# Optimization experiments

Hardware: AMD Instinct MI355X
Metric: run time of the kernel (lower is better)

## Reference

```python
import jax, jax.numpy as jnp
import numpy as np
from jax import lax

B = 2; C = 256; NH = 8; NP = 4; NUM_LAYERS = 6; FFN = 1024
IN_SIZES = (512, 1024, 2048)
LVL_SHAPES = ((64, 64), (32, 32), (16, 16), (8, 8), (4, 4))
NL = len(LVL_SHAPES); DH = C // NH
N = sum(h * w for h, w in LVL_SHAPES)  # 5456 tokens over the pyramid


def _ln(x, g, b):
    m = x.mean(-1, keepdims=True)
    v = x.var(-1, keepdims=True)
    return (x - m) * lax.rsqrt(v + 1e-5) * g + b


def _gn(x, g, b, groups=8):
    Bb, Cc, Hh, Ww = x.shape
    xr = x.reshape(Bb, groups, Cc // groups, Hh, Ww)
    m = xr.mean((2, 3, 4), keepdims=True)
    v = xr.var((2, 3, 4), keepdims=True)
    xr = (xr - m) * lax.rsqrt(v + 1e-5)
    return xr.reshape(Bb, Cc, Hh, Ww) * g[None, :, None, None] + b[None, :, None, None]


def _conv(x, w, b, stride, pad):
    y = lax.conv_general_dilated(x, w, (stride, stride), [(pad, pad), (pad, pad)],
                                 dimension_numbers=('NCHW', 'OIHW', 'NCHW'))
    return y + b[None, :, None, None]


def _priors():
    # normalized (cx, cy) anchor centers per pyramid location
    pr = []
    for (fh, fw) in LVL_SHAPES:
        cy = (jnp.arange(fh, dtype=jnp.float32) + 0.5) / fh
        cx = (jnp.arange(fw, dtype=jnp.float32) + 0.5) / fw
        gy, gx = jnp.meshgrid(cy, cx, indexing='ij')
        pr.append(jnp.stack([gx, gy], -1).reshape(-1, 2))
    return jnp.concatenate(pr, 0)  # [N,2]


def _sample(vl, loc, fh, fw):
    # vl: [B,NH,S_l,DH] flattened level values; loc: [B,N,NH,NP,2] in [0,1]
    x = loc[..., 0] * fw - 0.5
    y = loc[..., 1] * fh - 0.5
    x0 = jnp.floor(x); y0 = jnp.floor(y)
    lx = x - x0; ly = y - y0

    def gather(xi, yi):
        inb = ((xi >= 0) & (xi <= fw - 1) & (yi >= 0) & (yi <= fh - 1)).astype(vl.dtype)
        xc = jnp.clip(xi, 0, fw - 1).astype(jnp.int32)
        yc = jnp.clip(yi, 0, fh - 1).astype(jnp.int32)
        idx = (yc * fw + xc).transpose(0, 2, 1, 3).reshape(B, NH, N * NP)
        g = jnp.take_along_axis(vl, idx[..., None], axis=2)  # [B,NH,N*NP,DH]
        g = g.reshape(B, NH, N, NP, DH).transpose(0, 2, 1, 3, 4)  # [B,N,NH,NP,DH]
        return g * inb[..., None]

    return (gather(x0, y0) * ((1 - lx) * (1 - ly))[..., None]
            + gather(x0 + 1, y0) * (lx * (1 - ly))[..., None]
            + gather(x0, y0 + 1) * ((1 - lx) * ly)[..., None]
            + gather(x0 + 1, y0 + 1) * (lx * ly)[..., None])


def _attn_layer(x, priors, g1, b1_, woff, boff, watt, batt, wval, bval, wout, bout):
    q = _ln(x, g1, b1_)
    off = (q @ woff + boff).reshape(B, N, NH, NL, NP, 2)
    att = jax.nn.softmax((q @ watt + batt).reshape(B, N, NH, NL * NP), axis=-1)
    att = att.reshape(B, N, NH, NL, NP)
    val = (q @ wval + bval).reshape(B, N, NH, DH)
    normz = jnp.array([[w, h] for (h, w) in LVL_SHAPES], jnp.float32)  # (W,H) per level
    loc = priors[None, :, None, None, None, :] + off / normz[None, None, None, :, None, :]
    out = jnp.zeros((B, N, NH, DH), x.dtype)
    start = 0
    for l, (fh, fw) in enumerate(LVL_SHAPES):
        vl = val[:, start:start + fh * fw].transpose(0, 2, 1, 3)  # [B,NH,S_l,DH]
        s = _sample(vl, loc[:, :, :, l], fh, fw)  # [B,N,NH,NP,DH]
        out = out + (s * att[:, :, :, l, :, None]).sum(3)
        start += fh * fw
    return x + out.reshape(B, N, C) @ wout + bout


def _ffn(x, g2, b2_, w1, b1_, w2, b2_2):
    h = jax.nn.relu(_ln(x, g2, b2_) @ w1 + b1_)
    return x + h @ w2 + b2_2


def _forward(in_map0, in_map1, in_map2, pw0, pb0, pw1, pb1, pw2, pb2,
             buw0, bub0, gng, gnb, buw1, bub1,
             ln1g, ln1b, woff, boff, watt, batt, wval, bval, wout, bout,
             ln2g, ln2b, w1, b1, w2, b2):
    maps = [_conv(in_map0, pw0, pb0, 1, 0), _conv(in_map1, pw1, pb1, 1, 0), _conv(in_map2, pw2, pb2, 1, 0)]
    m = _conv(in_map2, buw0, bub0, 2, 1)  # bottom-up from raw C5 (2048ch)
    maps.append(m)
    m = _conv(jax.nn.relu(_gn(m, gng, gnb)), buw1, bub1, 2, 1)
    maps.append(m)
    feats = jnp.concatenate([mm.reshape(B, C, -1).transpose(0, 2, 1) for mm in maps], axis=1)  # [B,N,C]
    priors = _priors()
    for i in range(NUM_LAYERS):
        feats = _attn_layer(feats, priors, ln1g[i], ln1b[i], woff[i], boff[i],
                            watt[i], batt[i], wval[i], bval[i], wout[i], bout[i])
        feats = _ffn(feats, ln2g[i], ln2b[i], w1[i], b1[i], w2[i], b2[i])
    return feats


def setup_inputs():
    key = jax.random.key(0)
    ks = list(jax.random.split(key, 40)); ki = iter(ks)
    def rn(shape, s=0.02):
        return jax.random.normal(next(ki), shape, jnp.float32) * s
    inp = {}
    for i, (cs, (h, w)) in enumerate(zip(IN_SIZES, LVL_SHAPES[:3])):
        inp[f"in_map{i}"] = jax.random.normal(next(ki), (B, cs, h, w), jnp.float32)
    for i, cs in enumerate(IN_SIZES):
        inp[f"pw{i}"] = rn((C, cs, 1, 1)); inp[f"pb{i}"] = jnp.zeros((C,), jnp.float32)
    inp["buw0"] = rn((C, IN_SIZES[-1], 3, 3)); inp["bub0"] = jnp.zeros((C,), jnp.float32)
    inp["gng"] = jnp.ones((C,), jnp.float32); inp["gnb"] = jnp.zeros((C,), jnp.float32)
    inp["buw1"] = rn((C, C, 3, 3)); inp["bub1"] = jnp.zeros((C,), jnp.float32)
    LYR = NUM_LAYERS
    inp["ln1g"] = jnp.ones((LYR, C), jnp.float32); inp["ln1b"] = jnp.zeros((LYR, C), jnp.float32)
    inp["woff"] = rn((LYR, C, NH * NL * NP * 2), 0.01)
    th = np.arange(NH) * (2.0 * np.pi / NH)
    grid = np.stack([np.cos(th), np.sin(th)], -1)
    grid = grid / np.abs(grid).max(-1, keepdims=True)  # [NH,2]
    boff = np.tile(grid[:, None, None, :], (1, NL, NP, 1)) * (np.arange(NP) + 1)[None, None, :, None]
    inp["boff"] = jnp.tile(jnp.asarray(boff.reshape(-1), jnp.float32)[None], (LYR, 1))
    inp["watt"] = rn((LYR, C, NH * NL * NP), 0.01); inp["batt"] = jnp.zeros((LYR, NH * NL * NP), jnp.float32)
    inp["wval"] = rn((LYR, C, C)); inp["bval"] = jnp.zeros((LYR, C), jnp.float32)
    inp["wout"] = rn((LYR, C, C)); inp["bout"] = jnp.zeros((LYR, C), jnp.float32)
    inp["ln2g"] = jnp.ones((LYR, C), jnp.float32); inp["ln2b"] = jnp.zeros((LYR, C), jnp.float32)
    inp["w1"] = rn((LYR, C, FFN)); inp["b1"] = jnp.zeros((LYR, FFN), jnp.float32)
    inp["w2"] = rn((LYR, FFN, C)); inp["b2"] = jnp.zeros((LYR, C), jnp.float32)
    return inp


def reference(in_map0, in_map1, in_map2, pw0, pb0, pw1, pb1, pw2, pb2,
              buw0, bub0, gng, gnb, buw1, bub1,
              ln1g, ln1b, woff, boff, watt, batt, wval, bval, wout, bout,
              ln2g, ln2b, w1, b1, w2, b2):
    feats = _forward(in_map0, in_map1, in_map2, pw0, pb0, pw1, pb1, pw2, pb2,
                     buw0, bub0, gng, gnb, buw1, bub1,
                     ln1g, ln1b, woff, boff, watt, batt, wval, bval, wout, bout,
                     ln2g, ln2b, w1, b1, w2, b2)
    outs = []
    start = 0
    for (fh, fw) in LVL_SHAPES:
        outs.append(feats[:, start:start + fh * fw].transpose(0, 2, 1).reshape(B, C, fh, fw))
        start += fh * fw
    return tuple(outs)
```

## Files before the change

### kernel.cpp

```cpp
#include <hip/hip_runtime.h>
#include <cstdint>

typedef long long i64;
typedef unsigned short u16;
typedef __attribute__((ext_vector_type(8))) short short8;
typedef __attribute__((ext_vector_type(8))) unsigned short us8;
typedef __attribute__((ext_vector_type(4))) float f32x4;

#define NTOK 5456
#define BNROWS 10912
#define NLAYERS 6

__device__ __forceinline__ u16 f2bf(float f) {
  unsigned u = __float_as_uint(f);
  return (u16)((u + 0x7FFFu + ((u >> 16) & 1u)) >> 16);
}
__device__ __forceinline__ float bf2f(u16 h) {
  return __uint_as_float(((unsigned)h) << 16);
}

template<int BNT>
__global__ __launch_bounds__(256) void mgemm_k(
    const u16* __restrict__ A, const u16* __restrict__ B, int K,
    float* __restrict__ C, float* __restrict__ C2, u16* __restrict__ C16, i64 sCm,
    const float* __restrict__ bias, int relu, int addres, int qkv,
    int M, int N, int mbsh, i64 bCz,
    int KS, float* __restrict__ part)
{
  constexpr int NW = BNT / 32;
  __shared__ u16 Asm[2][128 * 64];
  __shared__ u16 Bsm[2][BNT * 64];
  int tid = threadIdx.x;

  int bx = blockIdx.x, by = blockIdx.y;
  int gx = gridDim.x, gy = gridDim.y;
  int nwg = gx * gy;
  if (KS == 1 && nwg >= 16) {
    int lin = bx + gx * by;
    int xcd = lin & 7, k = lin >> 3;
    int q = nwg >> 3, r = nwg & 7;
    int f = (xcd < r) ? (xcd * (q + 1) + k) : (r * (q + 1) + (xcd - r) * q + k);
    bx = f / gy;
    by = f - bx * gy;
  }
  int m0 = bx * 128, n0 = by * BNT;

  int ks = blockIdx.z;
  int Kc = K / KS;
  int k0 = ks * Kc;
  int lane = tid & 63, w = tid >> 6;
  int wr = w >> 1, wc = w & 1;
  int r16 = lane & 15, g = lane >> 4;

  f32x4 acc[4][NW];
#pragma unroll
  for (int mi = 0; mi < 4; mi++)
#pragma unroll
    for (int nj = 0; nj < NW; nj++) acc[mi][nj] = (f32x4){0.f, 0.f, 0.f, 0.f};

  const u16* Ag = A + (i64)m0 * K + k0;
  const u16* Bg = B + (i64)n0 * K + k0;
  int nt = Kc >> 6;

  auto stage = [&](int buf, int kt) {
#pragma unroll
    for (int r = 0; r < 4; r++) {
      int s = r * 256 + tid;
      int row = s >> 3, c = s & 7;
      int cs = ((c ^ (row & 7)) << 3);
      __builtin_amdgcn_global_load_lds(
          (const __attribute__((address_space(1))) void*)(Ag + (i64)row * K + kt + cs),
          (__attribute__((address_space(3))) void*)(&Asm[buf][(r * 256 + (w << 6)) << 3]),
          16, 0, 0);
    }
#pragma unroll
    for (int r = 0; r < NW; r++) {
      int s = r * 256 + tid;
      int row = s >> 3, c = s & 7;
      int cs = ((c ^ (row & 7)) << 3);
      __builtin_amdgcn_global_load_lds(
          (const __attribute__((address_space(1))) void*)(Bg + (i64)row * K + kt + cs),
          (__attribute__((address_space(3))) void*)(&Bsm[buf][(r * 256 + (w << 6)) << 3]),
          16, 0, 0);
    }
  };

  stage(0, 0);
  __syncthreads();
  for (int t = 0; t < nt; t++) {
    int cur = t & 1;
    if (t + 1 < nt) stage(cur ^ 1, (t + 1) << 6);
#pragma unroll
    for (int h = 0; h < 2; h++) {
      short8 av[4], bv[NW];
#pragma unroll
      for (int mi = 0; mi < 4; mi++) {
        int row = wr * 64 + mi * 16 + r16;
        av[mi] = *(const short8*)&Asm[cur][row * 64 + ((((h << 2) + g) ^ (row & 7)) << 3)];
      }
#pragma unroll
      for (int nj = 0; nj < NW; nj++) {
        int row = wc * (NW * 16) + nj * 16 + r16;
        bv[nj] = *(const short8*)&Bsm[cur][row * 64 + ((((h << 2) + g) ^ (row & 7)) << 3)];
      }
#pragma unroll
      for (int mi = 0; mi < 4; mi++)
#pragma unroll
        for (int nj = 0; nj < NW; nj++)
          acc[mi][nj] = __builtin_amdgcn_mfma_f32_16x16x32_bf16(
              av[mi], bv[nj], acc[mi][nj], 0, 0, 0);
    }
    __syncthreads();
  }

  if (KS > 1) {
#pragma unroll
    for (int mi = 0; mi < 4; mi++)
#pragma unroll
      for (int nj = 0; nj < NW; nj++)
#pragma unroll
        for (int r = 0; r < 4; r++) {
          int grow = m0 + wr * 64 + mi * 16 + g * 4 + r;
          int gcol = n0 + wc * (NW * 16) + nj * 16 + r16;
          if (grow < M) part[((i64)ks * M + grow) * N + gcol] = acc[mi][nj][r];
        }
  } else if (qkv) {
    u16* off16 = (u16*)C;
    u16* att16 = (u16*)C2;
#pragma unroll
    for (int mi = 0; mi < 4; mi++)
#pragma unroll
      for (int nj = 0; nj < NW; nj++)
#pragma unroll
        for (int r = 0; r < 4; r++) {
          int grow = m0 + wr * 64 + mi * 16 + g * 4 + r;
          int gcol = n0 + wc * (NW * 16) + nj * 16 + r16;
          if (grow < M) {
            float v = acc[mi][nj][r] + bias[gcol];
            if (gcol < 320) off16[(i64)grow * 320 + gcol] = f2bf(v);
            else if (gcol < 480) att16[(i64)grow * 160 + (gcol - 320)] = f2bf(v);
            else if (gcol < 736) C16[(i64)grow * 256 + (gcol - 480)] = f2bf(v);
          }
        }
  } else {
    float bv[NW];
    int gc0 = n0 + wc * (NW * 16) + r16;
#pragma unroll
    for (int nj = 0; nj < NW; nj++)
      bv[nj] = bias ? bias[gc0 + nj * 16] : 0.f;
    int mask = (1 << mbsh) - 1;
#pragma unroll
    for (int mi = 0; mi < 4; mi++) {
#pragma unroll
      for (int r = 0; r < 4; r++) {
        int grow = m0 + wr * 64 + mi * 16 + g * 4 + r;
        if (grow >= M) continue;
        i64 rowb = (i64)(grow >> mbsh) * bCz + (i64)(grow & mask) * sCm;
#pragma unroll
        for (int nj = 0; nj < NW; nj++) {
          int gcol = gc0 + nj * 16;
          if (gcol >= N) continue;
          float v = acc[mi][nj][r] + bv[nj];
          if (relu) v = fmaxf(v, 0.f);
          i64 ci = rowb + gcol;
          if (C16) C16[ci] = f2bf(v);
          else {
            if (addres) v += C[ci];
            C[ci] = v;
          }
        }
      }
    }
  }
}

__global__ __launch_bounds__(512, 1) void ffn_fused_k(
    float* __restrict__ feats, const u16* __restrict__ w1n,
    const u16* __restrict__ w2n, const float* __restrict__ b1,
    const float* __restrict__ b2, const float* __restrict__ lng,
    const float* __restrict__ lnb, int M)
{
  __shared__ u16 B1s[2][64 * 256];
  __shared__ u16 B2s[2][256 * 64];
  __shared__ u16 Hs[64 * 88];
  __shared__ float b1s[1024];
  u16* As = &B1s[1][0];

  int tid = threadIdx.x;
  int lane = tid & 63, w = tid >> 6;
  int wr = w >> 1, wc = w & 1;
  int r16 = lane & 15, g = lane >> 4;
  int m0 = blockIdx.x * 64;

  auto stageW = [&](int buf, int ch) {
#pragma unroll
    for (int r = 0; r < 4; r++) {
      int s = r * 512 + tid;
      int row = s >> 5, c = s & 31;
      int cs = ((c ^ (row & 7)) << 3);
      __builtin_amdgcn_global_load_lds(
          (const __attribute__((address_space(1))) void*)(w1n + (i64)(ch * 64 + row) * 256 + cs),
          (__attribute__((address_space(3))) void*)(&B1s[buf][(r * 512 + (w << 6)) << 3]),
          16, 0, 0);
    }
#pragma unroll
    for (int r = 0; r < 4; r++) {
      int s = r * 512 + tid;
      int row = s >> 3, c = s & 7;
      int cs = ((c ^ (row & 7)) << 3);
      __builtin_amdgcn_global_load_lds(
          (const __attribute__((address_space(1))) void*)(w2n + (i64)row * 1024 + ch * 64 + cs),
          (__attribute__((address_space(3))) void*)(&B2s[buf][(r * 512 + (w << 6)) << 3]),
          16, 0, 0);
    }
  };

  stageW(0, 0);
  for (int i = tid; i < 1024; i += 512) b1s[i] = b1[i];

  {
    int rw = tid >> 3, c0 = (tid & 7) * 32;
    const float* fr = feats + (i64)(m0 + rw) * 256 + c0;
    float4 x[8];
    float s = 0.f, ss = 0.f;
#pragma unroll
    for (int j = 0; j < 8; j++) {
      x[j] = ((const float4*)fr)[j];
      s += x[j].x + x[j].y + x[j].z + x[j].w;
      ss += x[j].x * x[j].x + x[j].y * x[j].y + x[j].z * x[j].z + x[j].w * x[j].w;
    }
#pragma unroll
    for (int o = 1; o <= 4; o <<= 1) { s += __shfl_xor(s, o); ss += __shfl_xor(ss, o); }
    float mean = s * (1.f / 256.f);
    float rs = rsqrtf(ss * (1.f / 256.f) - mean * mean + 1e-5f);
    const float4* gp = (const float4*)(lng + c0);
    const float4* bp = (const float4*)(lnb + c0);
#pragma unroll
    for (int j = 0; j < 8; j += 2) {
      float4 g0 = gp[j], g1 = gp[j + 1];
      float4 b0 = bp[j], b1_ = bp[j + 1];
      us8 o;
      o[0] = f2bf((x[j].x - mean) * rs * g0.x + b0.x);
      o[1] = f2bf((x[j].y - mean) * rs * g0.y + b0.y);
      o[2] = f2bf((x[j].z - mean) * rs * g0.z + b0.z);
      o[3] = f2bf((x[j].w - mean) * rs * g0.w + b0.w);
      o[4] = f2bf((x[j + 1].x - mean) * rs * g1.x + b1_.x);
      o[5] = f2bf((x[j + 1].y - mean) * rs * g1.y + b1_.y);
      o[6] = f2bf((x[j + 1].z - mean) * rs * g1.z + b1_.z);
      o[7] = f2bf((x[j + 1].w - mean) * rs * g1.w + b1_.w);
      int gr = (tid & 7) * 4 + (j >> 1);
      *(us8*)&As[rw * 256 + ((gr ^ (rw & 7)) << 3)] = o;
    }
  }
  __syncthreads();

  short8 av_all[8];
  {
    int row = wr * 16 + r16;
#pragma unroll
    for (int ks = 0; ks < 8; ks++)
      av_all[ks] = *(const short8*)&As[row * 256 + (((ks * 4 + g) ^ (row & 7)) << 3)];
  }
  __syncthreads();

  f32x4 acc2[8];
#pragma unroll
  for (int nj = 0; nj < 8; nj++) acc2[nj] = (f32x4){0.f, 0.f, 0.f, 0.f};

  int cur = 0;
  for (int ch = 0; ch < 16; ch++) {
    if (ch + 1 < 16) stageW(cur ^ 1, ch + 1);

    f32x4 acc1[2];
#pragma unroll
    for (int nj = 0; nj < 2; nj++) acc1[nj] = (f32x4){0.f, 0.f, 0.f, 0.f};
#pragma unroll
    for (int ks = 0; ks < 8; ks++) {
      short8 bv[2];
#pragma unroll
      for (int nj = 0; nj < 2; nj++) {
        int row = wc * 32 + nj * 16 + r16;
        bv[nj] = *(const short8*)&B1s[cur][row * 256 + (((ks * 4 + g) ^ (row & 7)) << 3)];
      }
#pragma unroll
      for (int nj = 0; nj < 2; nj++)
        acc1[nj] = __builtin_amdgcn_mfma_f32_16x16x32_bf16(
            av_all[ks], bv[nj], acc1[nj], 0, 0, 0);
    }
#pragma unroll
    for (int nj = 0; nj < 2; nj++)
#pragma unroll
      for (int r = 0; r < 4; r++) {
        int hr = wr * 16 + g * 4 + r;
        int hc = wc * 32 + nj * 16 + r16;
        float v = acc1[nj][r] + b1s[ch * 64 + hc];
        Hs[hr * 88 + hc] = f2bf(fmaxf(v, 0.f));
      }
    __syncthreads();

#pragma unroll
    for (int hh = 0; hh < 2; hh++) {
      short8 av2 = *(const short8*)&Hs[(wr * 16 + r16) * 88 + hh * 32 + g * 8];
      short8 bv2[8];
#pragma unroll
      for (int nj = 0; nj < 8; nj++) {
        int n = wc * 128 + nj * 16 + r16;
        bv2[nj] = *(const short8*)&B2s[cur][n * 64 + (((hh * 4 + g) ^ (n & 7)) << 3)];
      }
#pragma unroll
      for (int nj = 0; nj < 8; nj++)
        acc2[nj] = __builtin_amdgcn_mfma_f32_16x16x32_bf16(
            av2, bv2[nj], acc2[nj], 0, 0, 0);
    }
    __syncthreads();
    cur ^= 1;
  }

#pragma unroll
  for (int r = 0; r < 4; r++) {
    int grow = m0 + wr * 16 + g * 4 + r;
    if (grow >= M) continue;
#pragma unroll
    for (int nj = 0; nj < 8; nj++) {
      int col = wc * 128 + nj * 16 + r16;
      i64 ci = (i64)grow * 256 + col;
      feats[ci] += acc2[nj][r] + b2[col];
    }
  }
}

__global__ void reduce_k(const float* __restrict__ part, float* __restrict__ C,
    const float* __restrict__ bias, int mbsh, i64 bCz, i64 sCm, int M, int N, int KS)
{
  int idx = blockIdx.x * 256 + threadIdx.x;
  if (idx >= M * N) return;
  int m = idx / N, n = idx - m * N;
  float v = bias ? bias[n] : 0.f;
  for (int ks = 0; ks < KS; ks++) v += part[((i64)ks * M + m) * N + n];
  C[(i64)(m >> mbsh) * bCz + (i64)(m & ((1 << mbsh) - 1)) * sCm + n] = v;
}

__global__ void cvt_w_pro_k(const float* __restrict__ pw0, const float* __restrict__ pw1,
    const float* __restrict__ pw2, const float* __restrict__ buw0,
    const float* __restrict__ buw1, u16* __restrict__ dst)
{
  int idx = blockIdx.x * 256 + threadIdx.x;
  if (idx >= 6225920) return;
  float v;
  if (idx < 131072) v = pw0[idx];
  else if (idx < 393216) v = pw1[idx - 131072];
  else if (idx < 917504) v = pw2[idx - 393216];
  else if (idx < 5636096) v = buw0[idx - 917504];
  else v = buw1[idx - 5636096];
  dst[idx] = f2bf(v);
}

__global__ void cvt_w_layer_k(const float* __restrict__ woff, const float* __restrict__ watt,
    const float* __restrict__ wval, const float* __restrict__ wout,
    const float* __restrict__ w1, const float* __restrict__ w2, u16* __restrict__ dst)
{
  int L = blockIdx.y;
  int o = blockIdx.x * 256 + threadIdx.x;
  if (o >= 786432) return;
  u16* d = dst + (i64)L * 786432;
  float v;
  if (o < 196608) {
    int n = o >> 8, k = o & 255;
    if (n < 320) v = woff[(i64)L * 81920 + k * 320 + n];
    else if (n < 480) v = watt[(i64)L * 40960 + k * 160 + (n - 320)];
    else if (n < 736) v = wval[(i64)L * 65536 + k * 256 + (n - 480)];
    else v = 0.f;
  } else if (o < 262144) {
    int o2 = o - 196608; int n = o2 >> 8, k = o2 & 255;
    v = wout[(i64)L * 65536 + k * 256 + n];
  } else if (o < 524288) {
    int o2 = o - 262144; int n = o2 >> 8, k = o2 & 255;
    v = w1[(i64)L * 262144 + (i64)k * 1024 + n];
  } else {
    int o2 = o - 524288; int n = o2 >> 10, k = o2 & 1023;
    v = w2[(i64)L * 262144 + (i64)k * 256 + n];
  }
  d[o] = f2bf(v);
}

__global__ void cvt_bias_k(const float* __restrict__ boff, const float* __restrict__ batt,
    const float* __restrict__ bval, float* __restrict__ bq)
{
  int idx = blockIdx.x * 256 + threadIdx.x;
  if (idx >= NLAYERS * 768) return;
  int L = idx / 768, n = idx - L * 768;
  float v;
  if (n < 320) v = boff[(i64)L * 320 + n];
  else if (n < 480) v = batt[(i64)L * 160 + (n - 320)];
  else if (n < 736) v = bval[(i64)L * 256 + (n - 480)];
  else v = 0.f;
  bq[idx] = v;
}

__global__ __launch_bounds__(256) void trans_cvt_k(const float* __restrict__ in,
    u16* __restrict__ out, int K, int P)
{
  __shared__ float tile[32][33];
  int p0 = blockIdx.x * 32, k0 = blockIdx.y * 32, b = blockIdx.z;
  int tx = threadIdx.x & 31, ty = threadIdx.x >> 5;
  const float* ib = in + (i64)b * K * P;
  for (int i = ty; i < 32; i += 8)
    tile[i][tx] = ib[(i64)(k0 + i) * P + p0 + tx];
  __syncthreads();
  for (int i = ty; i < 32; i += 8)
    out[((i64)b * P + p0 + i) * K + k0 + tx] = f2bf(tile[tx][i]);
}

__global__ void im2col_bf16_k(const float* __restrict__ in, u16* __restrict__ out,
    int Cin, int Hin, int Win, int Ho, int Wo)
{
  int Kk = Cin * 9;
  i64 total = (i64)2 * Ho * Wo * Kk;
  i64 o = (i64)blockIdx.x * 256 + threadIdx.x;
  if (o >= total) return;
  int k = (int)(o % Kk);
  int m = (int)(o / Kk);
  int hw = Ho * Wo;
  int b = m / hw, pix = m - b * hw;
  int oy = pix / Wo, ox = pix - oy * Wo;
  int ci = k / 9, r = k - ci * 9;
  int ky = r / 3, kx = r - ky * 3;
  int iy = oy * 2 - 1 + ky, ix = ox * 2 - 1 + kx;
  float v = 0.f;
  if (iy >= 0 && iy < Hin && ix >= 0 && ix < Win)
    v = in[(((i64)b * Cin + ci) * Hin + iy) * Win + ix];
  out[o] = f2bf(v);
}

__global__ void gn_relu_k(const float* __restrict__ feats, float* __restrict__ y,
    const float* __restrict__ g, const float* __restrict__ bt)
{
  int grp = blockIdx.x, b = blockIdx.y;
  int tid = threadIdx.x;
  const float* fb = feats + ((i64)b * NTOK + 5376) * 256 + grp * 32;
  float s = 0.f, ss = 0.f;
  for (int i = tid; i < 2048; i += 256) {
    int cl = i >> 6, p = i & 63;
    float v = fb[(i64)p * 256 + cl];
    s += v; ss += v * v;
  }
  __shared__ float sb[4], ssb[4];
#pragma unroll
  for (int o = 32; o > 0; o >>= 1) { s += __shfl_down(s, o); ss += __shfl_down(ss, o); }
  int wv = tid >> 6;
  if ((tid & 63) == 0) { sb[wv] = s; ssb[wv] = ss; }
  __syncthreads();
  float ts = sb[0] + sb[1] + sb[2] + sb[3];
  float tss = ssb[0] + ssb[1] + ssb[2] + ssb[3];
  float mean = ts * (1.f / 2048.f);
  float rs = rsqrtf(tss * (1.f / 2048.f) - mean * mean + 1e-5f);
  for (int i = tid; i < 2048; i += 256) {
    int cl = i >> 6, p = i & 63;
    int c = grp * 32 + cl;
    float v = (fb[(i64)p * 256 + cl] - mean) * rs * g[c] + bt[c];
    y[((i64)b * 256 + c) * 64 + p] = fmaxf(v, 0.f);
  }
}

__global__ __launch_bounds__(256) void ln_k(const float* __restrict__ x,
    u16* __restrict__ y, const float* __restrict__ g, const float* __restrict__ bt,
    int rows)
{
  int row = blockIdx.x * 4 + (threadIdx.x >> 6);
  if (row >= rows) return;
  int lane = threadIdx.x & 63;
  float4 v = ((const float4*)(x + (i64)row * 256))[lane];
  float s = v.x + v.y + v.z + v.w;
  float ss = v.x * v.x + v.y * v.y + v.z * v.z + v.w * v.w;
#pragma unroll
  for (int o = 32; o > 0; o >>= 1) { s += __shfl_down(s, o); ss += __shfl_down(ss, o); }
  s = __shfl(s, 0);
  ss = __shfl(ss, 0);
  float mean = s * (1.f / 256.f);
  float rs = rsqrtf(ss * (1.f / 256.f) - mean * mean + 1e-5f);
  float4 gg = ((const float4*)g)[lane];
  float4 bb = ((const float4*)bt)[lane];
  ushort4 o4;
  o4.x = f2bf((v.x - mean) * rs * gg.x + bb.x);
  o4.y = f2bf((v.y - mean) * rs * gg.y + bb.y);
  o4.z = f2bf((v.z - mean) * rs * gg.z + bb.z);
  o4.w = f2bf((v.w - mean) * rs * gg.w + bb.w);
  ((ushort4*)(y + (i64)row * 256))[lane] = o4;
}

__global__ __launch_bounds__(256) void dsample_k(
    const u16* __restrict__ val, const u16* __restrict__ off,
    const u16* __restrict__ att, u16* __restrict__ out)
{
  const int FH[5] = {64, 32, 16, 8, 4};
  const int ST[5] = {0, 4096, 5120, 5376, 5440};
  int bid = blockIdx.x;
  int chunk = (bid & 7) * 86 + (bid >> 3);
  if (chunk >= 682) return;
  int lane = threadIdx.x & 63;
  int half = lane >> 5;
  int l32 = lane & 31;
  int t = chunk * 8 + ((threadIdx.x >> 6) << 1) + half;
  int b = blockIdx.y;
  int h = l32 >> 2, d4 = l32 & 3;

  int lv;
  if (t < 4096)      lv = 0;
  else if (t < 5120) lv = 1;
  else if (t < 5376) lv = 2;
  else if (t < 5440) lv = 3;
  else               lv = 4;
  int loc = t - ST[lv];
  int sh = 6 - lv;
  int py = loc >> sh, px = loc - (py << sh);
  float inv = 1.f / (float)FH[lv];
  float prx = (px + 0.5f) * inv, pry = (py + 0.5f) * inv;
  i64 bt = (i64)b * NTOK + t;
  const u16* offp = off + bt * 320 + h * 40;
  const u16* attp = att + bt * 160 + h * 20;
  const u16* vbase = val + ((i64)b * NTOK) * 256 + h * 32 + d4 * 8;

  float own_a[5], own_fx[5], own_fy[5];
  int own_pk[5];
  float mx = -1e30f;
#pragma unroll
  for (int j = 0; j < 5; j++) {
    float lg = bf2f(attp[d4 + 4 * j]);
    own_a[j] = lg;
    mx = fmaxf(mx, lg);
  }
  mx = fmaxf(mx, __shfl_xor(mx, 1));
  mx = fmaxf(mx, __shfl_xor(mx, 2));
  float sum = 0.f;
#pragma unroll
  for (int j = 0; j < 5; j++) {
    float e = __expf(own_a[j] - mx);
    own_a[j] = e;
    sum += e;
  }
  sum += __shfl_xor(sum, 1);
  sum += __shfl_xor(sum, 2);
  float rinv = 1.f / sum;
#pragma unroll
  for (int j = 0; j < 5; j++) {
    int p = d4 + 4 * j;
    own_a[j] *= rinv;
    unsigned opk = *(const unsigned*)(offp + 2 * p);
    float ox = bf2f((u16)(opk & 0xFFFF));
    float oy = bf2f((u16)(opk >> 16));
    float sff = (float)(64 >> j);
    float xx = prx * sff + ox - 0.5f;
    float yy = pry * sff + oy - 0.5f;
    float xf = floorf(xx), yf = floorf(yy);
    own_fx[j] = xx - xf;
    own_fy[j] = yy - yf;
    own_pk[j] = (((int)yf) << 16) | (((int)xf) & 0xFFFF);
  }

  float acc[8] = {0.f, 0.f, 0.f, 0.f, 0.f, 0.f, 0.f, 0.f};
#pragma unroll
  for (int p = 0; p < 20; p++) {
    const int j = p >> 2;
    const int sf = FH[j], st = ST[j];
    int src = (half << 5) | (h << 2) | (p & 3);
    float wa = __shfl(own_a[j], src);
    float fx = __shfl(own_fx[j], src);
    float fy = __shfl(own_fy[j], src);
    int pk = __shfl(own_pk[j], src);
    int x0 = (pk << 16) >> 16;
    int y0 = pk >> 16;
    float gx0 = wa - wa * fx, gx1 = wa * fx;
    float w00 = gx0 - gx0 * fy, w01 = gx0 * fy;
    float w10 = gx1 - gx1 * fy, w11 = gx1 * fy;
    bool xin0 = (x0 >= 0) & (x0 < sf), xin1 = (x0 + 1 >= 0) & (x0 + 1 < sf);
    bool yin0 = (y0 >= 0) & (y0 < sf), yin1 = (y0 + 1 >= 0) & (y0 + 1 < sf);
    int ibase = st + y0 * sf + x0;
#define FMA8(W, IDX) { \
      us8 v = *(const us8*)(vbase + (i64)(IDX) * 256); \
      acc[0] = fmaf(W, bf2f(v[0]), acc[0]); acc[1] = fmaf(W, bf2f(v[1]), acc[1]); \
      acc[2] = fmaf(W, bf2f(v[2]), acc[2]); acc[3] = fmaf(W, bf2f(v[3]), acc[3]); \
      acc[4] = fmaf(W, bf2f(v[4]), acc[4]); acc[5] = fmaf(W, bf2f(v[5]), acc[5]); \
      acc[6] = fmaf(W, bf2f(v[6]), acc[6]); acc[7] = fmaf(W, bf2f(v[7]), acc[7]); }
    if (xin0 & yin0) FMA8(w00, ibase);
    if (xin1 & yin0) FMA8(w10, ibase + 1);
    if (xin0 & yin1) FMA8(w01, ibase + sf);
    if (xin1 & yin1) FMA8(w11, ibase + sf + 1);
#undef FMA8
  }
  us8 o;
#pragma unroll
  for (int i = 0; i < 8; i++) o[i] = f2bf(acc[i]);
  *(us8*)(out + ((bt * 8 + h) * 32 + d4 * 8)) = o;
}

__global__ __launch_bounds__(256) void untranspose_all_k(
    const float* __restrict__ feats, float* __restrict__ out)
{
  int u = blockIdx.x;
  int pt0, start, S; i64 ooff;
  if (u < 128)      { pt0 = u;       start = 0;    S = 4096; ooff = 0; }
  else if (u < 160) { pt0 = u - 128; start = 4096; S = 1024; ooff = 2097152; }
  else if (u < 168) { pt0 = u - 160; start = 5120; S = 256;  ooff = 2621440; }
  else if (u < 170) { pt0 = u - 168; start = 5376; S = 64;   ooff = 2752512; }
  else              { pt0 = 0;       start = 5440; S = 16;   ooff = 2785280; }
  __shared__ float tile[32][33];
  int pt = pt0 * 32, ct = blockIdx.y * 32, b = blockIdx.z;
  int tx = threadIdx.x & 31, ty = threadIdx.x >> 5;
  for (int i = ty; i < 32; i += 8) {
    int p = pt + i;
    tile[i][tx] = (p < S) ? feats[((i64)b * NTOK + start + p) * 256 + ct + tx] : 0.f;
  }
  __syncthreads();
  for (int i = ty; i < 32; i += 8) {
    int c = ct + i, p = pt + tx;
    if (p < S) out[ooff + ((i64)b * 256 + c) * S + p] = tile[tx][i];
  }
}

extern "C" void kernel_launch(void* const* d_in, const int* in_sizes, int n_in,
                              void* d_out, int out_size, void* d_ws, size_t ws_size,
                              hipStream_t stream)
{
  const float* in0  = (const float*)d_in[0];
  const float* in1  = (const float*)d_in[1];
  const float* in2  = (const float*)d_in[2];
  const float* pw0  = (const float*)d_in[3];
  const float* pb0  = (const float*)d_in[4];
  const float* pw1  = (const float*)d_in[5];
  const float* pb1  = (const float*)d_in[6];
  const float* pw2  = (const float*)d_in[7];
  const float* pb2  = (const float*)d_in[8];
  const float* buw0 = (const float*)d_in[9];
  const float* bub0 = (const float*)d_in[10];
  const float* gng  = (const float*)d_in[11];
  const float* gnb  = (const float*)d_in[12];
  const float* buw1 = (const float*)d_in[13];
  const float* bub1 = (const float*)d_in[14];
  const float* ln1g = (const float*)d_in[15];
  const float* ln1b = (const float*)d_in[16];
  const float* woff = (const float*)d_in[17];
  const float* boff = (const float*)d_in[18];
  const float* watt = (const float*)d_in[19];
  const float* batt = (const float*)d_in[20];
  const float* wval = (const float*)d_in[21];
  const float* bval = (const float*)d_in[22];
  const float* wout = (const float*)d_in[23];
  const float* bout = (const float*)d_in[24];
  const float* ln2g = (const float*)d_in[25];
  const float* ln2b = (const float*)d_in[26];
  const float* w1   = (const float*)d_in[27];
  const float* b1   = (const float*)d_in[28];
  const float* w2   = (const float*)d_in[29];
  const float* b2   = (const float*)d_in[30];
  float* out = (float*)d_out;

  const i64 TC = (i64)NTOK * 256;

  float* ws    = (float*)d_ws;
  float* feats = ws;
  u16*   qb    = (u16*)(feats + 2793472);
  u16*   valb  = qb + 2818048;
  u16*   sampb = valb + 2818048;
  float* U     = (float*)(sampb + 2818048);
  u16*   off16 = (u16*)U;
  u16*   att16 = off16 + 3491840;
  u16*   abuf  = (u16*)U;
  float* part  = U + 2097152;
  u16*   wb    = (u16*)(U + 5637120);
  float* bqkv  = (float*)(wb + 10944512);
  float* m4gn  = bqkv + 4608;

  auto mg128 = [&](dim3 grid, const u16* A, const u16* B, int K,
                   float* C, float* C2, u16* C16, i64 sCm, const float* bias,
                   int relu, int addres, int qkv, int M, int N, int mbsh, i64 bCz, int KS) {
    mgemm_k<128><<<grid, dim3(256), 0, stream>>>(A, B, K, C, C2, C16, sCm, bias,
        relu, addres, qkv, M, N, mbsh, bCz, KS, part);
  };
  auto mg64 = [&](dim3 grid, const u16* A, const u16* B, int K,
                  float* C, u16* C16, i64 sCm, const float* bias,
                  int relu, int addres, int M, int N, int mbsh, i64 bCz, int KS) {
    mgemm_k<64><<<grid, dim3(256), 0, stream>>>(A, B, K, C, nullptr, C16, sCm, bias,
        relu, addres, 0, M, N, mbsh, bCz, KS, part);
  };

  cvt_w_pro_k<<<dim3(24320), dim3(256), 0, stream>>>(pw0, pw1, pw2, buw0, buw1, wb);
  cvt_w_layer_k<<<dim3(3072, NLAYERS), dim3(256), 0, stream>>>(
      woff, watt, wval, wout, w1, w2, wb + 6225920);
  cvt_bias_k<<<dim3(18), dim3(256), 0, stream>>>(boff, batt, bval, bqkv);

  trans_cvt_k<<<dim3(128, 16, 2), dim3(256), 0, stream>>>(in0, abuf, 512, 4096);
  mg64(dim3(64, 4, 1), abuf, wb, 512, feats, nullptr, 256, pb0, 0, 0,
       8192, 256, 12, TC, 1);
  trans_cvt_k<<<dim3(32, 32, 2), dim3(256), 0, stream>>>(in1, abuf, 1024, 1024);
  mg64(dim3(16, 4, 2), abuf, wb + 131072, 1024, nullptr, nullptr, 256, nullptr, 0, 0,
       2048, 256, 10, 0, 2);
  reduce_k<<<dim3(2048), dim3(256), 0, stream>>>(part, feats + (i64)4096 * 256, pb1,
      10, TC, 256, 2048, 256, 2);
  trans_cvt_k<<<dim3(8, 64, 2), dim3(256), 0, stream>>>(in2, abuf, 2048, 256);
  mg64(dim3(4, 4, 4), abuf, wb + 393216, 2048, nullptr, nullptr, 256, nullptr, 0, 0,
       512, 256, 8, 0, 4);
  reduce_k<<<dim3(512), dim3(256), 0, stream>>>(part, feats + (i64)5120 * 256, pb2,
      8, TC, 256, 512, 256, 4);

  im2col_bf16_k<<<dim3(9216), dim3(256), 0, stream>>>(in2, abuf, 2048, 16, 16, 8, 8);
  mg64(dim3(1, 4, 16), abuf, wb + 917504, 18432, nullptr, nullptr, 256, nullptr, 0, 0,
       128, 256, 6, 0, 16);
  reduce_k<<<dim3(128), dim3(256), 0, stream>>>(part, feats + (i64)5376 * 256, bub0,
      6, TC, 256, 128, 256, 16);

  gn_relu_k<<<dim3(8, 2), dim3(256), 0, stream>>>(feats, m4gn, gng, gnb);
  im2col_bf16_k<<<dim3(288), dim3(256), 0, stream>>>(m4gn, abuf, 256, 8, 8, 4, 4);
  mg64(dim3(1, 4, 4), abuf, wb + 5636096, 2304, nullptr, nullptr, 256, nullptr, 0, 0,
       32, 256, 4, 0, 4);
  reduce_k<<<dim3(32), dim3(256), 0, stream>>>(part, feats + (i64)5440 * 256, bub1,
      4, TC, 256, 32, 256, 4);

  for (int i = 0; i < NLAYERS; i++) {
    const u16* wbL = wb + 6225920 + (i64)i * 786432;
    ln_k<<<dim3(2728), dim3(256), 0, stream>>>(feats, qb,
        ln1g + (i64)i * 256, ln1b + (i64)i * 256, BNROWS);
    mg128(dim3(86, 6, 1), qb, wbL, 256, (float*)off16, (float*)att16, valb, 0,
          bqkv + (i64)i * 768, 0, 0, 1, BNROWS, 768, 14, 0, 1);
    dsample_k<<<dim3(688, 2), dim3(256), 0, stream>>>(valb, off16, att16, sampb);
    mg64(dim3(86, 4, 1), sampb, wbL + 196608, 256, feats, nullptr, 256,
         bout + (i64)i * 256, 0, 1, BNROWS, 256, 14, 0, 1);
    ffn_fused_k<<<dim3(171), dim3(512), 0, stream>>>(feats, wbL + 262144,
        wbL + 524288, b1 + (i64)i * 1024, b2 + (i64)i * 256,
        ln2g + (i64)i * 256, ln2b + (i64)i * 256, BNROWS);
  }

  untranspose_all_k<<<dim3(171, 8, 2), dim3(256), 0, stream>>>(feats, out);
  (void)in_sizes; (void)n_in; (void)out_size; (void)ws_size;
}
```

Measured before the change: 935.8 us.

## Merge weight conversions, drop split-K reduce for level1, use 64-wide tiles for QKV

Merges the three weight and bias conversion kernels into one launch that dispatches on block index. The level-1 projection GEMM now writes directly with its bias instead of going through split-K partials and a reduce kernel. The per-layer QKV projection GEMM moves from the 128-column tile variant to the 64-column variant with twice as many column blocks. These changes cut launch count and raise block-level parallelism on the QKV GEMM, at the cost of less B-tile reuse per block there.

After: 884.4 us. -5.5%, faster.

```diff
diff --git a/kernel.cpp b/kernel.cpp
--- a/kernel.cpp
+++ b/kernel.cpp
@@ -340,61 +340,62 @@
   C[(i64)(m >> mbsh) * bCz + (i64)(m & ((1 << mbsh) - 1)) * sCm + n] = v;
 }
 
-__global__ void cvt_w_pro_k(const float* __restrict__ pw0, const float* __restrict__ pw1,
+__global__ void cvt_all_k(const float* __restrict__ pw0, const float* __restrict__ pw1,
     const float* __restrict__ pw2, const float* __restrict__ buw0,
-    const float* __restrict__ buw1, u16* __restrict__ dst)
-{
-  int idx = blockIdx.x * 256 + threadIdx.x;
-  if (idx >= 6225920) return;
-  float v;
-  if (idx < 131072) v = pw0[idx];
-  else if (idx < 393216) v = pw1[idx - 131072];
-  else if (idx < 917504) v = pw2[idx - 393216];
-  else if (idx < 5636096) v = buw0[idx - 917504];
-  else v = buw1[idx - 5636096];
-  dst[idx] = f2bf(v);
-}
-
-__global__ void cvt_w_layer_k(const float* __restrict__ woff, const float* __restrict__ watt,
+    const float* __restrict__ buw1,
+    const float* __restrict__ woff, const float* __restrict__ watt,
     const float* __restrict__ wval, const float* __restrict__ wout,
-    const float* __restrict__ w1, const float* __restrict__ w2, u16* __restrict__ dst)
-{
-  int L = blockIdx.y;
-  int o = blockIdx.x * 256 + threadIdx.x;
-  if (o >= 786432) return;
-  u16* d = dst + (i64)L * 786432;
-  float v;
-  if (o < 196608) {
-    int n = o >> 8, k = o & 255;
-    if (n < 320) v = woff[(i64)L * 81920 + k * 320 + n];
-    else if (n < 480) v = watt[(i64)L * 40960 + k * 160 + (n - 320)];
-    else if (n < 736) v = wval[(i64)L * 65536 + k * 256 + (n - 480)];
-    else v = 0.f;
-  } else if (o < 262144) {
-    int o2 = o - 196608; int n = o2 >> 8, k = o2 & 255;
-    v = wout[(i64)L * 65536 + k * 256 + n];
-  } else if (o < 524288) {
-    int o2 = o - 262144; int n = o2 >> 8, k = o2 & 255;
-    v = w1[(i64)L * 262144 + (i64)k * 1024 + n];
+    const float* __restrict__ w1, const float* __restrict__ w2,
+    const float* __restrict__ boff, const float* __restrict__ batt,
+    const float* __restrict__ bval,
+    u16* __restrict__ wb, float* __restrict__ bq)
+{
+  int blk = blockIdx.x;
+  if (blk < 24320) {
+    int idx = blk * 256 + threadIdx.x;
+    if (idx >= 6225920) return;
+    float v;
+    if (idx < 131072) v = pw0[idx];
+    else if (idx < 393216) v = pw1[idx - 131072];
+    else if (idx < 917504) v = pw2[idx - 393216];
+    else if (idx < 5636096) v = buw0[idx - 917504];
+    else v = buw1[idx - 5636096];
+    wb[idx] = f2bf(v);
+  } else if (blk < 24320 + 18432) {
+    int lb = blk - 24320;
+    int L = lb / 3072;
+    int o = (lb - L * 3072) * 256 + threadIdx.x;
+    if (o >= 786432) return;
+    u16* d = wb + 6225920 + (i64)L * 786432;
+    float v;
+    if (o < 196608) {
+      int n = o >> 8, k = o & 255;
+      if (n < 320) v = woff[(i64)L * 81920 + k * 320 + n];
+      else if (n < 480) v = watt[(i64)L * 40960 + k * 160 + (n - 320)];
+      else if (n < 736) v = wval[(i64)L * 65536 + k * 256 + (n - 480)];
+      else v = 0.f;
+    } else if (o < 262144) {
+      int o2 = o - 196608; int n = o2 >> 8, k = o2 & 255;
+      v = wout[(i64)L * 65536 + k * 256 + n];
+    } else if (o < 524288) {
+      int o2 = o - 262144; int n = o2 >> 8, k = o2 & 255;
+      v = w1[(i64)L * 262144 + (i64)k * 1024 + n];
+    } else {
+      int o2 = o - 524288; int n = o2 >> 10, k = o2 & 1023;
+      v = w2[(i64)L * 262144 + (i64)k * 256 + n];
+    }
+    d[o] = f2bf(v);
   } else {
-    int o2 = o - 524288; int n = o2 >> 10, k = o2 & 1023;
-    v = w2[(i64)L * 262144 + (i64)k * 256 + n];
-  }
-  d[o] = f2bf(v);
-}
-
-__global__ void cvt_bias_k(const float* __restrict__ boff, const float* __restrict__ batt,
-    const float* __restrict__ bval, float* __restrict__ bq)
-{
-  int idx = blockIdx.x * 256 + threadIdx.x;
-  if (idx >= NLAYERS * 768) return;
-  int L = idx / 768, n = idx - L * 768;
-  float v;
-  if (n < 320) v = boff[(i64)L * 320 + n];
-  else if (n < 480) v = batt[(i64)L * 160 + (n - 320)];
-  else if (n < 736) v = bval[(i64)L * 256 + (n - 480)];
-  else v = 0.f;
-  bq[idx] = v;
+    for (int idx = threadIdx.x; idx < NLAYERS * 768; idx += 256) {
+      int L = idx / 768, n = idx - L * 768;
+      float v;
+      if (n < 320) v = boff[(i64)L * 320 + n];
+      else if (n < 480) v = batt[(i64)L * 160 + (n - 320)];
+      else if (n < 736) v = bval[(i64)L * 256 + (n - 480)];
+      else v = 0.f;
+      bq[idx] = v;
+    }
+  }
 }
 
 __global__ __launch_bounds__(256) void trans_cvt_k(const float* __restrict__ in,
@@ -677,41 +678,38 @@
         relu, addres, qkv, M, N, mbsh, bCz, KS, part);
   };
   auto mg64 = [&](dim3 grid, const u16* A, const u16* B, int K,
-                  float* C, u16* C16, i64 sCm, const float* bias,
-                  int relu, int addres, int M, int N, int mbsh, i64 bCz, int KS) {
-    mgemm_k<64><<<grid, dim3(256), 0, stream>>>(A, B, K, C, nullptr, C16, sCm, bias,
-        relu, addres, 0, M, N, mbsh, bCz, KS, part);
+                  float* C, float* C2, u16* C16, i64 sCm, const float* bias,
+                  int relu, int addres, int qkv, int M, int N, int mbsh, i64 bCz, int KS) {
+    mgemm_k<64><<<grid, dim3(256), 0, stream>>>(A, B, K, C, C2, C16, sCm, bias,
+        relu, addres, qkv, M, N, mbsh, bCz, KS, part);
   };
 
-  cvt_w_pro_k<<<dim3(24320), dim3(256), 0, stream>>>(pw0, pw1, pw2, buw0, buw1, wb);
-  cvt_w_layer_k<<<dim3(3072, NLAYERS), dim3(256), 0, stream>>>(
-      woff, watt, wval, wout, w1, w2, wb + 6225920);
-  cvt_bias_k<<<dim3(18), dim3(256), 0, stream>>>(boff, batt, bval, bqkv);
+  cvt_all_k<<<dim3(24320 + 18432 + 1), dim3(256), 0, stream>>>(
+      pw0, pw1, pw2, buw0, buw1, woff, watt, wval, wout, w1, w2,
+      boff, batt, bval, wb, bqkv);
 
   trans_cvt_k<<<dim3(128, 16, 2), dim3(256), 0, stream>>>(in0, abuf, 512, 4096);
-  mg64(dim3(64, 4, 1), abuf, wb, 512, feats, nullptr, 256, pb0, 0, 0,
+  mg64(dim3(64, 4, 1), abuf, wb, 512, feats, nullptr, nullptr, 256, pb0, 0, 0, 0,
        8192, 256, 12, TC, 1);
   trans_cvt_k<<<dim3(32, 32, 2), dim3(256), 0, stream>>>(in1, abuf, 1024, 1024);
-  mg64(dim3(16, 4, 2), abuf, wb + 131072, 1024, nullptr, nullptr, 256, nullptr, 0, 0,
-       2048, 256, 10, 0, 2);
-  reduce_k<<<dim3(2048), dim3(256), 0, stream>>>(part, feats + (i64)4096 * 256, pb1,
-      10, TC, 256, 2048, 256, 2);
+  mg64(dim3(16, 4, 1), abuf, wb + 131072, 1024, feats + (i64)4096 * 256, nullptr,
+       nullptr, 256, pb1, 0, 0, 0, 2048, 256, 10, TC, 1);
   trans_cvt_k<<<dim3(8, 64, 2), dim3(256), 0, stream>>>(in2, abuf, 2048, 256);
-  mg64(dim3(4, 4, 4), abuf, wb + 393216, 2048, nullptr, nullptr, 256, nullptr, 0, 0,
-       512, 256, 8, 0, 4);
+  mg64(dim3(4, 4, 4), abuf, wb + 393216, 2048, nullptr, nullptr, nullptr, 256,
+       nullptr, 0, 0, 0, 512, 256, 8, 0, 4);
   reduce_k<<<dim3(512), dim3(256), 0, stream>>>(part, feats + (i64)5120 * 256, pb2,
       8, TC, 256, 512, 256, 4);
 
   im2col_bf16_k<<<dim3(9216), dim3(256), 0, stream>>>(in2, abuf, 2048, 16, 16, 8, 8);
-  mg64(dim3(1, 4, 16), abuf, wb + 917504, 18432, nullptr, nullptr, 256, nullptr, 0, 0,
-       128, 256, 6, 0, 16);
+  mg64(dim3(1, 4, 16), abuf, wb + 917504, 18432, nullptr, nullptr, nullptr, 256,
+       nullptr, 0, 0, 0, 128, 256, 6, 0, 16);
   reduce_k<<<dim3(128), dim3(256), 0, stream>>>(part, feats + (i64)5376 * 256, bub0,
       6, TC, 256, 128, 256, 16);
 
   gn_relu_k<<<dim3(8, 2), dim3(256), 0, stream>>>(feats, m4gn, gng, gnb);
   im2col_bf16_k<<<dim3(288), dim3(256), 0, stream>>>(m4gn, abuf, 256, 8, 8, 4, 4);
-  mg64(dim3(1, 4, 4), abuf, wb + 5636096, 2304, nullptr, nullptr, 256, nullptr, 0, 0,
-       32, 256, 4, 0, 4);
+  mg64(dim3(1, 4, 4), abuf, wb + 5636096, 2304, nullptr, nullptr, nullptr, 256,
+       nullptr, 0, 0, 0, 32, 256, 4, 0, 4);
   reduce_k<<<dim3(32), dim3(256), 0, stream>>>(part, feats + (i64)5440 * 256, bub1,
       4, TC, 256, 32, 256, 4);
 
@@ -719,11 +717,11 @@
     const u16* wbL = wb + 6225920 + (i64)i * 786432;
     ln_k<<<dim3(2728), dim3(256), 0, stream>>>(feats, qb,
         ln1g + (i64)i * 256, ln1b + (i64)i * 256, BNROWS);
-    mg128(dim3(86, 6, 1), qb, wbL, 256, (float*)off16, (float*)att16, valb, 0,
-          bqkv + (i64)i * 768, 0, 0, 1, BNROWS, 768, 14, 0, 1);
+    mg64(dim3(86, 12, 1), qb, wbL, 256, (float*)off16, (float*)att16, valb, 0,
+         bqkv + (i64)i * 768, 0, 0, 1, BNROWS, 768, 14, 0, 1);
     dsample_k<<<dim3(688, 2), dim3(256), 0, stream>>>(valb, off16, att16, sampb);
-    mg64(dim3(86, 4, 1), sampb, wbL + 196608, 256, feats, nullptr, 256,
-         bout + (i64)i * 256, 0, 1, BNROWS, 256, 14, 0, 1);
+    mg64(dim3(86, 4, 1), sampb, wbL + 196608, 256, feats, nullptr, nullptr, 256,
+         bout + (i64)i * 256, 0, 1, 0, BNROWS, 256, 14, 0, 1);
     ffn_fused_k<<<dim3(171), dim3(512), 0, stream>>>(feats, wbL + 262144,
         wbL + 524288, b1 + (i64)i * 1024, b2 + (i64)i * 256,
         ln2g + (i64)i * 256, ln2b + (i64)i * 256, BNROWS);
```
